# Optimization experiments

Measured on AMD Instinct MI355X. Metric: run time of the kernel, lower is better.

Reference implementation:

```python
import jax, jax.numpy as jnp
import numpy as np

D_MODEL = 768
D_STATE = 128
EXPAND = 2
D_CONV = 4
HEADDIM = 48
D_INNER = EXPAND * D_MODEL            # 1536
NHEADS = D_INNER // HEADDIM           # 32
CONV_DIM = D_INNER + 2 * D_STATE      # 1792 (ngroups=1)
D_IN_PROJ = 2 * D_INNER + 2 * D_STATE + NHEADS  # 3360
EPS = 1e-5


def setup_inputs() -> dict:
    key = jax.random.key(0)
    ks = jax.random.split(key, 8)
    B, L = 2, 1024
    x = jax.random.normal(ks[0], (B, L, D_MODEL), dtype=jnp.float32)
    in_proj_w = jax.random.normal(ks[1], (D_IN_PROJ, D_MODEL), dtype=jnp.float32) * 0.02
    conv_w = jax.random.normal(ks[2], (CONV_DIM, D_CONV), dtype=jnp.float32) * 0.1
    conv_b = jnp.zeros((CONV_DIM,), dtype=jnp.float32)
    # dt init as in Mamba2: dt ~ logspace[1e-3, 1e-1], dt_bias = softplus^-1(dt)
    u = jax.random.uniform(ks[3], (NHEADS,), dtype=jnp.float32)
    dt = jnp.exp(u * (np.log(0.1) - np.log(0.001)) + np.log(0.001))
    dt_bias = jnp.log(jnp.expm1(dt))
    # A in [1, 16]
    A_log = jnp.log(jax.random.uniform(ks[4], (NHEADS,), dtype=jnp.float32) * 15.0 + 1.0)
    D = jnp.ones((NHEADS,), dtype=jnp.float32)
    rms_w = jnp.ones((D_INNER,), dtype=jnp.float32)
    out_proj_w = jax.random.normal(ks[5], (D_MODEL, D_INNER), dtype=jnp.float32) * 0.02
    ln_w = jnp.ones((D_MODEL,), dtype=jnp.float32)
    ln_b = jnp.zeros((D_MODEL,), dtype=jnp.float32)
    return {"x": x, "in_proj_w": in_proj_w, "conv_w": conv_w, "conv_b": conv_b,
            "dt_bias": dt_bias, "A_log": A_log, "D": D, "rms_w": rms_w,
            "out_proj_w": out_proj_w, "ln_w": ln_w, "ln_b": ln_b}


def _mamba_block(x, in_proj_w, conv_w, conv_b, dt_bias, A_log, D, rms_w, out_proj_w, ln_w, ln_b):
    B, L, _ = x.shape
    zxbcdt = jnp.einsum('bld,ed->ble', x, in_proj_w)          # (B,L,D_IN_PROJ)
    z = zxbcdt[..., :D_INNER]                                  # gate
    xBC = zxbcdt[..., D_INNER:D_INNER + CONV_DIM]              # (B,L,CONV_DIM)
    dt = jax.nn.softplus(zxbcdt[..., -NHEADS:] + dt_bias)      # (B,L,H)

    # causal depthwise conv1d (kernel 4) + SiLU
    xp = jnp.pad(xBC, ((0, 0), (D_CONV - 1, 0), (0, 0)))
    conv = conv_b
    for k in range(D_CONV):
        conv = conv + xp[:, k:k + L, :] * conv_w[:, k]
    xBC = jax.nn.silu(conv)

    xs = xBC[..., :D_INNER].reshape(B, L, NHEADS, HEADDIM)     # (B,L,H,P)
    Bm = xBC[..., D_INNER:D_INNER + D_STATE]                   # (B,L,N)
    Cm = xBC[..., D_INNER + D_STATE:]                          # (B,L,N)

    A = -jnp.exp(A_log)                                        # (H,)
    dA = jnp.exp(dt * A)                                       # (B,L,H)
    xdt = xs * dt[..., None]                                   # (B,L,H,P)

    def step(h, inp):
        dA_t, xdt_t, B_t, C_t = inp                            # (B,H),(B,H,P),(B,N),(B,N)
        h = h * dA_t[:, :, None, None] + jnp.einsum('bhp,bn->bhpn', xdt_t, B_t)
        y_t = jnp.einsum('bhpn,bn->bhp', h, C_t)
        return h, y_t

    h0 = jnp.zeros((B, NHEADS, HEADDIM, D_STATE), dtype=x.dtype)
    _, ys = jax.lax.scan(step, h0,
                         (dA.transpose(1, 0, 2), xdt.transpose(1, 0, 2, 3),
                          Bm.transpose(1, 0, 2), Cm.transpose(1, 0, 2)))
    y = ys.transpose(1, 0, 2, 3) + D[None, None, :, None] * xs  # (B,L,H,P)
    y = y.reshape(B, L, D_INNER)

    # gated RMSNorm: rmsnorm(y * silu(z)) * rms_w
    yg = y * jax.nn.silu(z)
    yg = yg * jax.lax.rsqrt(jnp.mean(yg * yg, axis=-1, keepdims=True) + EPS) * rms_w
    out = jnp.einsum('ble,de->bld', yg, out_proj_w)

    # residual + LayerNorm
    r = out + x
    mu = jnp.mean(r, axis=-1, keepdims=True)
    var = jnp.mean((r - mu) ** 2, axis=-1, keepdims=True)
    return (r - mu) * jax.lax.rsqrt(var + EPS) * ln_w + ln_b


def reference(x, in_proj_w, conv_w, conv_b, dt_bias, A_log, D, rms_w, out_proj_w, ln_w, ln_b):
    return _mamba_block(x, in_proj_w, conv_w, conv_b, dt_bias, A_log, D, rms_w,
                        out_proj_w, ln_w, ln_b)
```

## Files before the change

### kernel.cpp

```cpp
#include <hip/hip_runtime.h>
#include <math.h>

#define BDIM 2
#define LLEN 1024
#define DMODEL 768
#define DINNER 1536
#define DSTATE 128
#define NH 32
#define HD 48
#define CONVD 1792
#define DPROJ 3360
#define DPROJP 3456
#define QCH 128
#define NCH 8
#define ROWS (BDIM*LLEN)

typedef unsigned short ushort_t;
typedef __attribute__((ext_vector_type(4))) short short4v;
typedef __attribute__((ext_vector_type(8))) short short8v;
typedef __attribute__((ext_vector_type(4))) float floatx4;

#define OFF_ZX   0ull
#define OFF_XBC  3538944ull
#define OFF_DT   5373952ull
#define OFF_LA   5439488ull
#define OFF_SC   5505024ull
#define OFF_Y    8650752ull
#define OFF_PP   10223616ull
#define OFF_CBT  10224640ull
#define OFF_BTBF 10486784ull
#define OFF_XPT  10617856ull
#define OFF_XBF  12190720ull
#define OFF_IPW  12977152ull
#define OFF_OPW  14304256ull
#define OFF_YBF  14894080ull
#define OFF_GO   16466944ull

__device__ __forceinline__ ushort_t f2bf(float f) {
  union { float f; unsigned int u; } v; v.f = f;
  return (ushort_t)((v.u + 0x7FFFu + ((v.u >> 16) & 1u)) >> 16);
}
__device__ __forceinline__ float bf2f(short s) {
  union { unsigned int u; float f; } v; v.u = ((unsigned int)(ushort_t)s) << 16;
  return v.f;
}

#define GLOAD_LDS16(gptr, lptr) \
  __builtin_amdgcn_global_load_lds( \
      (const __attribute__((address_space(1))) void*)(gptr), \
      (__attribute__((address_space(3))) void*)(lptr), 16, 0, 0)

__global__ __launch_bounds__(256) void convert_in_kernel(
    const float* __restrict__ x, const float* __restrict__ w,
    const float* __restrict__ opw, ushort_t* __restrict__ xbf,
    ushort_t* __restrict__ ipwbf, ushort_t* __restrict__ opwbf) {
  const int blk = blockIdx.x;
  if (blk < 768) {
    const int i = blk * 256 + threadIdx.x;
    const float4 a = ((const float4*)x)[i * 2];
    const float4 b = ((const float4*)x)[i * 2 + 1];
    short8v o;
    o[0] = (short)f2bf(a.x); o[1] = (short)f2bf(a.y);
    o[2] = (short)f2bf(a.z); o[3] = (short)f2bf(a.w);
    o[4] = (short)f2bf(b.x); o[5] = (short)f2bf(b.y);
    o[6] = (short)f2bf(b.z); o[7] = (short)f2bf(b.w);
    *(short8v*)(xbf + (size_t)i * 8) = o;
  } else if (blk < 2064) {
    const int i = (blk - 768) * 256 + threadIdx.x;
    const int row = i / (DMODEL / 8);
    short8v o;
    if (row < DPROJ) {
      const float4 a = ((const float4*)w)[i * 2];
      const float4 b = ((const float4*)w)[i * 2 + 1];
      o[0] = (short)f2bf(a.x); o[1] = (short)f2bf(a.y);
      o[2] = (short)f2bf(a.z); o[3] = (short)f2bf(a.w);
      o[4] = (short)f2bf(b.x); o[5] = (short)f2bf(b.y);
      o[6] = (short)f2bf(b.z); o[7] = (short)f2bf(b.w);
    } else {
      for (int j = 0; j < 8; j++) o[j] = 0;
    }
    *(short8v*)(ipwbf + (size_t)i * 8) = o;
  } else {
    const int i = (blk - 2064) * 256 + threadIdx.x;
    const float4 a = ((const float4*)opw)[i * 2];
    const float4 b = ((const float4*)opw)[i * 2 + 1];
    short8v o;
    o[0] = (short)f2bf(a.x); o[1] = (short)f2bf(a.y);
    o[2] = (short)f2bf(a.z); o[3] = (short)f2bf(a.w);
    o[4] = (short)f2bf(b.x); o[5] = (short)f2bf(b.y);
    o[6] = (short)f2bf(b.z); o[7] = (short)f2bf(b.w);
    *(short8v*)(opwbf + (size_t)i * 8) = o;
  }
}

__global__ __launch_bounds__(256) void gemm_bf16_bfout(
    const ushort_t* __restrict__ A, const ushort_t* __restrict__ B,
    ushort_t* __restrict__ C, int M, int N, int K) {
  __shared__ __align__(16) ushort_t As[128 * 32];
  __shared__ __align__(16) ushort_t Bs[128 * 32];
  const int tid = threadIdx.x, lane = tid & 63, w = tid >> 6;
  const int wm = (w >> 1) * 64, wn = (w & 1) * 64;
  const int m0 = blockIdx.y * 128, n0 = blockIdx.x * 128;
  floatx4 acc[4][4];
#pragma unroll
  for (int i = 0; i < 4; i++)
#pragma unroll
    for (int j = 0; j < 4; j++) acc[i][j] = (floatx4){0.f, 0.f, 0.f, 0.f};
  const int srow = tid >> 2, skc = (tid & 3) * 8;
  const int kk = (lane >> 4) * 8, fr = lane & 15;
  for (int k0 = 0; k0 < K; k0 += 32) {
#pragma unroll
    for (int i = 0; i < 2; i++) {
      GLOAD_LDS16(A + (size_t)(m0 + i * 64 + srow) * K + k0 + skc,
                  As + (i * 64 + srow) * 32 + skc);
      GLOAD_LDS16(B + (size_t)(n0 + i * 64 + srow) * K + k0 + skc,
                  Bs + (i * 64 + srow) * 32 + skc);
    }
    __syncthreads();
    short8v a[4], bv[4];
#pragma unroll
    for (int mr = 0; mr < 4; mr++)
      a[mr] = *(const short8v*)(As + (wm + mr * 16 + fr) * 32 + kk);
#pragma unroll
    for (int nc = 0; nc < 4; nc++)
      bv[nc] = *(const short8v*)(Bs + (wn + nc * 16 + fr) * 32 + kk);
#pragma unroll
    for (int mr = 0; mr < 4; mr++)
#pragma unroll
      for (int nc = 0; nc < 4; nc++)
        acc[mr][nc] = __builtin_amdgcn_mfma_f32_16x16x32_bf16(
            a[mr], bv[nc], acc[mr][nc], 0, 0, 0);
    __syncthreads();
  }
  const int crow = (lane >> 4) * 4;
#pragma unroll
  for (int mr = 0; mr < 4; mr++)
#pragma unroll
    for (int nc = 0; nc < 4; nc++)
#pragma unroll
      for (int j = 0; j < 4; j++)
        C[(size_t)(m0 + wm + mr * 16 + crow + j) * N + n0 + wn + nc * 16 + fr] =
            f2bf(acc[mr][nc][j]);
}

__global__ __launch_bounds__(256) void gemm_bf16_n64(
    const ushort_t* __restrict__ A, const ushort_t* __restrict__ B,
    float* __restrict__ C, int M, int N, int K) {
  __shared__ __align__(16) ushort_t As[128 * 32];
  __shared__ __align__(16) ushort_t Bs[64 * 32];
  const int tid = threadIdx.x, lane = tid & 63, w = tid >> 6;
  const int wm = (w >> 1) * 64, wn = (w & 1) * 32;
  const int m0 = blockIdx.y * 128, n0 = blockIdx.x * 64;
  floatx4 acc[4][2];
#pragma unroll
  for (int i = 0; i < 4; i++)
#pragma unroll
    for (int j = 0; j < 2; j++) acc[i][j] = (floatx4){0.f, 0.f, 0.f, 0.f};
  const int srow = tid >> 2, skc = (tid & 3) * 8;
  const int kk = (lane >> 4) * 8, fr = lane & 15;
  for (int k0 = 0; k0 < K; k0 += 32) {
#pragma unroll
    for (int i = 0; i < 2; i++)
      GLOAD_LDS16(A + (size_t)(m0 + i * 64 + srow) * K + k0 + skc,
                  As + (i * 64 + srow) * 32 + skc);
    GLOAD_LDS16(B + (size_t)(n0 + srow) * K + k0 + skc, Bs + srow * 32 + skc);
    __syncthreads();
    short8v a[4], bv[2];
#pragma unroll
    for (int mr = 0; mr < 4; mr++)
      a[mr] = *(const short8v*)(As + (wm + mr * 16 + fr) * 32 + kk);
#pragma unroll
    for (int nc = 0; nc < 2; nc++)
      bv[nc] = *(const short8v*)(Bs + (wn + nc * 16 + fr) * 32 + kk);
#pragma unroll
    for (int mr = 0; mr < 4; mr++)
#pragma unroll
      for (int nc = 0; nc < 2; nc++)
        acc[mr][nc] = __builtin_amdgcn_mfma_f32_16x16x32_bf16(
            a[mr], bv[nc], acc[mr][nc], 0, 0, 0);
    __syncthreads();
  }
  const int crow = (lane >> 4) * 4;
#pragma unroll
  for (int mr = 0; mr < 4; mr++)
#pragma unroll
    for (int nc = 0; nc < 2; nc++)
#pragma unroll
      for (int j = 0; j < 4; j++)
        C[(size_t)(m0 + wm + mr * 16 + crow + j) * N + n0 + wn + nc * 16 + fr] =
            acc[mr][nc][j];
}

__global__ __launch_bounds__(256) void conv_dt_kernel(
    const ushort_t* __restrict__ zxb, const float* __restrict__ conv_w,
    const float* __restrict__ conv_b, const float* __restrict__ dt_bias,
    ushort_t* __restrict__ xbcb, float* __restrict__ dtbuf) {
  const int row = blockIdx.x;
  const int t = row % LLEN;
  const int tid = threadIdx.x;
  for (int g = tid; g < CONVD / 4; g += 256) {
    const int c = g * 4;
    const float4 cb = *(const float4*)&conv_b[c];
    float acc0 = cb.x, acc1 = cb.y, acc2 = cb.z, acc3 = cb.w;
    float4 cw[4];
#pragma unroll
    for (int j = 0; j < 4; j++) cw[j] = *(const float4*)&conv_w[(c + j) * 4];
#pragma unroll
    for (int k = 0; k < 4; k++) {
      if (t - 3 + k >= 0) {
        const short4v v = *(const short4v*)&zxb[(size_t)(row - 3 + k) * DPROJP + DINNER + c];
        acc0 += bf2f(v[0]) * ((const float*)&cw[0])[k];
        acc1 += bf2f(v[1]) * ((const float*)&cw[1])[k];
        acc2 += bf2f(v[2]) * ((const float*)&cw[2])[k];
        acc3 += bf2f(v[3]) * ((const float*)&cw[3])[k];
      }
    }
    short4v o;
    o[0] = (short)f2bf(acc0 / (1.f + expf(-acc0)));
    o[1] = (short)f2bf(acc1 / (1.f + expf(-acc1)));
    o[2] = (short)f2bf(acc2 / (1.f + expf(-acc2)));
    o[3] = (short)f2bf(acc3 / (1.f + expf(-acc3)));
    *(short4v*)&xbcb[(size_t)row * CONVD + c] = o;
  }
  if (tid < NH) {
    const float v = bf2f(zxb[(size_t)row * DPROJP + (DPROJ - NH) + tid]) + dt_bias[tid];
    dtbuf[row * NH + tid] = (v > 20.f) ? v : log1pf(expf(v));
  }
}

__global__ __launch_bounds__(256) void prepfuse_kernel(
    const ushort_t* __restrict__ xbcb, const float* __restrict__ dtb,
    const float* __restrict__ A_log, ushort_t* __restrict__ XpT,
    ushort_t* __restrict__ BTbf, float* __restrict__ la2,
    float* __restrict__ Pp) {
  __shared__ ushort_t lb[128][136];
  __shared__ float dts[128];
  const int blk = blockIdx.x;
  const int tid = threadIdx.x;
  if (blk < 512) {
    const int c = blk & 7, h = (blk >> 3) & 31, b = blk >> 8;
    const int row0 = b * LLEN + c * QCH;
    if (tid < 128) dts[tid] = dtb[(size_t)(row0 + tid) * NH + h];
    __syncthreads();
    for (int idx = tid; idx < 128 * 12; idx += 256) {
      const int r = idx / 12, f4 = (idx % 12) * 4;
      const short4v v = *(const short4v*)&xbcb[(size_t)(row0 + r) * CONVD + h * HD + f4];
      const float d = dts[r];
      short4v o;
      o[0] = (short)f2bf(bf2f(v[0]) * d); o[1] = (short)f2bf(bf2f(v[1]) * d);
      o[2] = (short)f2bf(bf2f(v[2]) * d); o[3] = (short)f2bf(bf2f(v[3]) * d);
      *(short4v*)&lb[r][f4] = o;
    }
    __syncthreads();
    const size_t base = ((size_t)(b * NCH + c) * NH + h) * HD * 128;
    for (int idx = tid; idx < 48 * 16; idx += 256) {
      const int p = idx % 48, t0 = (idx / 48) * 8;
      short8v o;
#pragma unroll
      for (int j = 0; j < 8; j++) o[j] = lb[t0 + j][p];
      *(short8v*)&XpT[base + (size_t)p * 128 + t0] = o;
    }
  } else if (blk < 528) {
    const int bc = blk - 512;
    const int b = bc / NCH, c = bc % NCH;
    const int row0 = b * LLEN + c * QCH;
    for (int idx = tid; idx < 128 * 32; idx += 256) {
      const int t = idx >> 5, f4 = (idx & 31) * 4;
      const short4v v = *(const short4v*)&xbcb[(size_t)(row0 + t) * CONVD + DINNER + f4];
      *(short4v*)&lb[t][f4] = v;
    }
    __syncthreads();
    for (int idx = tid; idx < 128 * 16; idx += 256) {
      const int n = idx & 127, t0 = (idx >> 7) * 8;
      short8v o;
#pragma unroll
      for (int j = 0; j < 8; j++) o[j] = lb[t0 + j][n];
      *(short8v*)&BTbf[(size_t)(bc * 128 + n) * 128 + t0] = o;
    }
  } else {
    const int idx = blk - 528;
    const int c = idx & 7, h = (idx >> 3) & 31, b = idx >> 8;
    const int lane = tid & 63;
    const int row = b * LLEN + c * QCH + tid;
    float v = 0.f;
    if (tid < 128) v = dtb[(size_t)row * NH + h];
#pragma unroll
    for (int off = 1; off < 64; off <<= 1) {
      const float u = __shfl_up(v, off, 64);
      if (lane >= off) v += u;
    }
    if (tid == 63) dts[0] = v;
    __syncthreads();
    if (tid >= 64 && tid < 128) v += dts[0];
    if (tid < 128) {
      const float la2v = -expf(A_log[h]) * v * 1.44269504088896f;
      la2[(size_t)row * NH + h] = la2v;
      if (tid == 127) Pp[(b * NH + h) * NCH + c] = exp2f(la2v);
    }
  }
}

__global__ __launch_bounds__(256) void stateA_cbt_kernel(
    const ushort_t* __restrict__ XpT, const ushort_t* __restrict__ BTbf,
    const ushort_t* __restrict__ xbcb, const float* __restrict__ la2,
    float* __restrict__ Sc, float* __restrict__ CBt) {
  __shared__ float ew[128];
  const int blk = blockIdx.x;
  const int tid = threadIdx.x, lane = tid & 63, w = tid >> 6;
  const int fr = lane & 15, kk = (lane >> 4) * 8;
  if (blk < 512) {
    const int c = blk & 7, h = (blk >> 3) & 31, b = blk >> 8;
    const int bc = b * NCH + c, bh = b * NH + h;
    const int row0 = b * LLEN + c * QCH;
    const float laL = la2[(size_t)(row0 + 127) * NH + h];
    if (tid < 128) ew[tid] = exp2f(laL - la2[(size_t)(row0 + tid) * NH + h]);
    __syncthreads();
    const int wn = w * 32;
    const size_t xbase = ((size_t)bc * NH + h) * HD * 128;
    floatx4 acc[3][2];
#pragma unroll
    for (int i = 0; i < 3; i++)
#pragma unroll
      for (int j = 0; j < 2; j++) acc[i][j] = (floatx4){0.f, 0.f, 0.f, 0.f};
    for (int ki = 0; ki < 4; ki++) {
      const int kg = ki * 32 + kk;
      short8v a[3], bv[2];
#pragma unroll
      for (int mt = 0; mt < 3; mt++) {
        const short8v raw = *(const short8v*)&XpT[xbase + (size_t)(mt * 16 + fr) * 128 + kg];
        short8v s;
#pragma unroll
        for (int e = 0; e < 8; e++) s[e] = (short)f2bf(bf2f(raw[e]) * ew[kg + e]);
        a[mt] = s;
      }
#pragma unroll
      for (int nt = 0; nt < 2; nt++)
        bv[nt] = *(const short8v*)&BTbf[(size_t)(bc * 128 + wn + nt * 16 + fr) * 128 + kg];
#pragma unroll
      for (int mt = 0; mt < 3; mt++)
#pragma unroll
        for (int nt = 0; nt < 2; nt++)
          acc[mt][nt] = __builtin_amdgcn_mfma_f32_16x16x32_bf16(
              a[mt], bv[nt], acc[mt][nt], 0, 0, 0);
    }
    const int crow = (lane >> 4) * 4;
    float* sc = Sc + (size_t)(bh * NCH + c) * (HD * DSTATE);
#pragma unroll
    for (int mt = 0; mt < 3; mt++)
#pragma unroll
      for (int nt = 0; nt < 2; nt++)
#pragma unroll
        for (int j = 0; j < 4; j++)
          sc[(size_t)(mt * 16 + crow + j) * 128 + wn + nt * 16 + fr] = acc[mt][nt][j];
  } else {
    const int bc = blk - 512;
    const int b = bc / NCH, c = bc % NCH;
    const int row0 = b * LLEN + c * QCH;
    const int wm = w * 32;
    floatx4 acc[2][8];
#pragma unroll
    for (int i = 0; i < 2; i++)
#pragma unroll
      for (int j = 0; j < 8; j++) acc[i][j] = (floatx4){0.f, 0.f, 0.f, 0.f};
    for (int ki = 0; ki < 4; ki++) {
      const int kg = ki * 32 + kk;
      short8v a[2], bv[8];
#pragma unroll
      for (int mt = 0; mt < 2; mt++)
        a[mt] = *(const short8v*)&xbcb[(size_t)(row0 + wm + mt * 16 + fr) * CONVD +
                                       DINNER + DSTATE + kg];
#pragma unroll
      for (int nt = 0; nt < 8; nt++)
        bv[nt] = *(const short8v*)&xbcb[(size_t)(row0 + nt * 16 + fr) * CONVD +
                                        DINNER + kg];
#pragma unroll
      for (int mt = 0; mt < 2; mt++)
#pragma unroll
        for (int nt = 0; nt < 8; nt++)
          acc[mt][nt] = __builtin_amdgcn_mfma_f32_16x16x32_bf16(
              a[mt], bv[nt], acc[mt][nt], 0, 0, 0);
    }
    const int crow = (lane >> 4) * 4;
#pragma unroll
    for (int mt = 0; mt < 2; mt++)
#pragma unroll
      for (int nt = 0; nt < 8; nt++)
#pragma unroll
        for (int j = 0; j < 4; j++)
          CBt[(size_t)(bc * 128 + wm + mt * 16 + crow + j) * 128 + nt * 16 + fr] =
              acc[mt][nt][j];
  }
}

__global__ __launch_bounds__(256) void chunk_combine_kernel(
    float* __restrict__ Sc, const float* __restrict__ Pp) {
  const int bh = blockIdx.x >> 3;
  const int slice = blockIdx.x & 7;
  const int tid = threadIdx.x;
  const int e0 = slice * 768;
  for (int e = e0 + tid; e < e0 + 768; e += 256) {
    float hv = 0.f;
#pragma unroll
    for (int c = 0; c < NCH; c++) {
      const size_t idx = ((size_t)(bh * NCH + c)) * HD * DSTATE + e;
      const float sv = Sc[idx];
      Sc[idx] = hv;
      hv = hv * Pp[bh * NCH + c] + sv;
    }
  }
}

__global__ __launch_bounds__(256) void ykernel(
    const float* __restrict__ CBt, const ushort_t* __restrict__ XpT,
    const ushort_t* __restrict__ xbcb, const float* __restrict__ Hc,
    const float* __restrict__ la2, ushort_t* __restrict__ yb) {
  const int c = blockIdx.x, h = blockIdx.y, b = blockIdx.z;
  const int bc = b * NCH + c, bh = b * NH + h;
  const int row0 = b * LLEN + c * QCH;
  const int tid = threadIdx.x, lane = tid & 63, w = tid >> 6;
  __shared__ float laL[128], el[128];
  if (tid < 128) {
    const float v = la2[(size_t)(row0 + tid) * NH + h];
    laL[tid] = v; el[tid] = exp2f(v);
  }
  __syncthreads();
  const int wm = w * 32;
  const int fr = lane & 15, kk = (lane >> 4) * 8;
  const size_t xbase = ((size_t)bc * NH + h) * HD * 128;
  const float* hin = Hc + (size_t)(bh * NCH + c) * (HD * DSTATE);
  floatx4 acc[2][3];
#pragma unroll
  for (int i = 0; i < 2; i++)
#pragma unroll
    for (int j = 0; j < 3; j++) acc[i][j] = (floatx4){0.f, 0.f, 0.f, 0.f};

  for (int ki = 0; ki < 4; ki++) {
    const int kg = ki * 32 + kk;
    short8v a[2], bv[3];
#pragma unroll
    for (int mt = 0; mt < 2; mt++) {
      const int t = wm + mt * 16 + fr;
      const float lt = laL[t];
      const float* cb = &CBt[(size_t)(bc * 128 + t) * 128 + kg];
      const float4 u0 = *(const float4*)cb;
      const float4 u1 = *(const float4*)(cb + 4);
      const float f[8] = {u0.x, u0.y, u0.z, u0.w, u1.x, u1.y, u1.z, u1.w};
      short8v s;
#pragma unroll
      for (int e = 0; e < 8; e++) {
        const int sidx = kg + e;
        const float m = (t >= sidx) ? exp2f(lt - laL[sidx]) : 0.f;
        s[e] = (short)f2bf(f[e] * m);
      }
      a[mt] = s;
    }
#pragma unroll
    for (int nt = 0; nt < 3; nt++)
      bv[nt] = *(const short8v*)&XpT[xbase + (size_t)(nt * 16 + fr) * 128 + kg];
#pragma unroll
    for (int mt = 0; mt < 2; mt++)
#pragma unroll
      for (int nt = 0; nt < 3; nt++)
        acc[mt][nt] = __builtin_amdgcn_mfma_f32_16x16x32_bf16(
            a[mt], bv[nt], acc[mt][nt], 0, 0, 0);
  }
  for (int ki = 0; ki < 4; ki++) {
    const int kg = ki * 32 + kk;
    short8v a[2], bv[3];
#pragma unroll
    for (int mt = 0; mt < 2; mt++) {
      const int t = wm + mt * 16 + fr;
      const float scl = el[t];
      const short8v raw = *(const short8v*)&xbcb[(size_t)(row0 + t) * CONVD +
                                                 DINNER + DSTATE + kg];
      short8v s;
#pragma unroll
      for (int e = 0; e < 8; e++) s[e] = (short)f2bf(bf2f(raw[e]) * scl);
      a[mt] = s;
    }
#pragma unroll
    for (int nt = 0; nt < 3; nt++) {
      const float* hp = &hin[(size_t)(nt * 16 + fr) * 128 + kg];
      const float4 u0 = *(const float4*)hp;
      const float4 u1 = *(const float4*)(hp + 4);
      const float f[8] = {u0.x, u0.y, u0.z, u0.w, u1.x, u1.y, u1.z, u1.w};
      short8v s;
#pragma unroll
      for (int e = 0; e < 8; e++) s[e] = (short)f2bf(f[e]);
      bv[nt] = s;
    }
#pragma unroll
    for (int mt = 0; mt < 2; mt++)
#pragma unroll
      for (int nt = 0; nt < 3; nt++)
        acc[mt][nt] = __builtin_amdgcn_mfma_f32_16x16x32_bf16(
            a[mt], bv[nt], acc[mt][nt], 0, 0, 0);
  }
  const int crow = (lane >> 4) * 4;
#pragma unroll
  for (int mt = 0; mt < 2; mt++)
#pragma unroll
    for (int nt = 0; nt < 3; nt++)
#pragma unroll
      for (int j = 0; j < 4; j++) {
        const int row = row0 + wm + mt * 16 + crow + j;
        yb[(size_t)row * DINNER + h * HD + nt * 16 + fr] = f2bf(acc[mt][nt][j]);
      }
}

__global__ __launch_bounds__(256) void gate_rms_kernel(
    const ushort_t* __restrict__ zxb, const ushort_t* __restrict__ xbcb,
    const float* __restrict__ Dv, const float* __restrict__ rms_w,
    const ushort_t* __restrict__ yb, ushort_t* __restrict__ ybf) {
  const int row = blockIdx.x;
  const int tid = threadIdx.x;
  __shared__ float sred[4];
  float g[8];
  float ss = 0.f;
  if (tid < 192) {
    const int e0 = tid * 8;
    const short8v xv = *(const short8v*)&xbcb[(size_t)row * CONVD + e0];
    const short8v zv = *(const short8v*)&zxb[(size_t)row * DPROJP + e0];
    const short8v yv = *(const short8v*)&yb[(size_t)row * DINNER + e0];
#pragma unroll
    for (int j = 0; j < 8; j++) {
      const int e = e0 + j;
      const float yf = bf2f(yv[j]) + Dv[e / HD] * bf2f(xv[j]);
      const float z = bf2f(zv[j]);
      const float gv = yf * (z / (1.f + expf(-z)));
      g[j] = gv;
      ss += gv * gv;
    }
  } else {
#pragma unroll
    for (int j = 0; j < 8; j++) g[j] = 0.f;
  }
#pragma unroll
  for (int off = 32; off; off >>= 1) ss += __shfl_down(ss, off, 64);
  if ((tid & 63) == 0) sred[tid >> 6] = ss;
  __syncthreads();
  const float tot = sred[0] + sred[1] + sred[2] + sred[3];
  const float scale = rsqrtf(tot / DINNER + 1e-5f);
  if (tid < 192) {
    const int e0 = tid * 8;
    const float4 w0 = *(const float4*)&rms_w[e0];
    const float4 w1 = *(const float4*)&rms_w[e0 + 4];
    const float wf[8] = {w0.x, w0.y, w0.z, w0.w, w1.x, w1.y, w1.z, w1.w};
    short8v o;
#pragma unroll
    for (int j = 0; j < 8; j++) o[j] = (short)f2bf(g[j] * scale * wf[j]);
    *(short8v*)&ybf[(size_t)row * DINNER + e0] = o;
  }
}

__global__ __launch_bounds__(256) void resid_ln_kernel(
    const float* __restrict__ go, const float* __restrict__ x,
    const float* __restrict__ ln_w, const float* __restrict__ ln_b,
    float* __restrict__ out) {
  const int row = blockIdx.x;
  const int tid = threadIdx.x;
  __shared__ float sred[4];
  __shared__ float sred2[4];
  float r[3];
  float s = 0.f;
#pragma unroll
  for (int i = 0; i < 3; i++) {
    const int e = tid + i * 256;
    r[i] = go[(size_t)row * DMODEL + e] + x[(size_t)row * DMODEL + e];
    s += r[i];
  }
#pragma unroll
  for (int off = 32; off; off >>= 1) s += __shfl_down(s, off, 64);
  if ((tid & 63) == 0) sred[tid >> 6] = s;
  __syncthreads();
  const float mu = (sred[0] + sred[1] + sred[2] + sred[3]) * (1.f / DMODEL);
  float s2 = 0.f;
#pragma unroll
  for (int i = 0; i < 3; i++) {
    const float d = r[i] - mu;
    s2 += d * d;
  }
#pragma unroll
  for (int off = 32; off; off >>= 1) s2 += __shfl_down(s2, off, 64);
  if ((tid & 63) == 0) sred2[tid >> 6] = s2;
  __syncthreads();
  const float var = (sred2[0] + sred2[1] + sred2[2] + sred2[3]) * (1.f / DMODEL);
  const float inv = rsqrtf(var + 1e-5f);
#pragma unroll
  for (int i = 0; i < 3; i++) {
    const int e = tid + i * 256;
    out[(size_t)row * DMODEL + e] = (r[i] - mu) * inv * ln_w[e] + ln_b[e];
  }
}

extern "C" void kernel_launch(void* const* d_in, const int* in_sizes, int n_in,
                              void* d_out, int out_size, void* d_ws, size_t ws_size,
                              hipStream_t stream) {
  const float* x          = (const float*)d_in[0];
  const float* in_proj_w  = (const float*)d_in[1];
  const float* conv_w     = (const float*)d_in[2];
  const float* conv_b     = (const float*)d_in[3];
  const float* dt_bias    = (const float*)d_in[4];
  const float* A_log      = (const float*)d_in[5];
  const float* Dv         = (const float*)d_in[6];
  const float* rms_w      = (const float*)d_in[7];
  const float* out_proj_w = (const float*)d_in[8];
  const float* ln_w       = (const float*)d_in[9];
  const float* ln_b       = (const float*)d_in[10];
  float* out = (float*)d_out;
  float* ws  = (float*)d_ws;

  ushort_t* zxb   = (ushort_t*)(ws + OFF_ZX);
  ushort_t* xbcb  = (ushort_t*)(ws + OFF_XBC);
  float* dtb  = ws + OFF_DT;
  float* la2  = ws + OFF_LA;
  float* Sc   = ws + OFF_SC;
  ushort_t* ybuf = (ushort_t*)(ws + OFF_Y);
  float* Pp   = ws + OFF_PP;
  float* CBt  = ws + OFF_CBT;
  ushort_t* BTbf  = (ushort_t*)(ws + OFF_BTBF);
  ushort_t* XpT   = (ushort_t*)(ws + OFF_XPT);
  ushort_t* xbf   = (ushort_t*)(ws + OFF_XBF);
  ushort_t* ipwbf = (ushort_t*)(ws + OFF_IPW);
  ushort_t* opwbf = (ushort_t*)(ws + OFF_OPW);
  ushort_t* ybf   = (ushort_t*)(ws + OFF_YBF);
  float*    go    = ws + OFF_GO;

  convert_in_kernel<<<2640, 256, 0, stream>>>(x, in_proj_w, out_proj_w,
                                              xbf, ipwbf, opwbf);
  gemm_bf16_bfout<<<dim3(DPROJP / 128, ROWS / 128), 256, 0, stream>>>(
      xbf, ipwbf, zxb, ROWS, DPROJP, DMODEL);
  conv_dt_kernel<<<ROWS, 256, 0, stream>>>(zxb, conv_w, conv_b, dt_bias, xbcb, dtb);
  prepfuse_kernel<<<1040, 256, 0, stream>>>(xbcb, dtb, A_log, XpT, BTbf, la2, Pp);
  stateA_cbt_kernel<<<528, 256, 0, stream>>>(XpT, BTbf, xbcb, la2, Sc, CBt);
  chunk_combine_kernel<<<512, 256, 0, stream>>>(Sc, Pp);
  ykernel<<<dim3(NCH, NH, BDIM), 256, 0, stream>>>(CBt, XpT, xbcb, Sc, la2, ybuf);
  gate_rms_kernel<<<ROWS, 256, 0, stream>>>(zxb, xbcb, Dv, rms_w, ybuf, ybf);
  gemm_bf16_n64<<<dim3(DMODEL / 64, ROWS / 128), 256, 0, stream>>>(
      ybf, opwbf, go, ROWS, DMODEL, DINNER);
  resid_ln_kernel<<<ROWS, 256, 0, stream>>>(go, x, ln_w, ln_b, out);
}
```

Before: 210.0 us.

## Fuse chunk-state combine into ykernel, store CB in bf16, resize blocks

Removes the separate chunk_combine kernel. Each ykernel block now rebuilds its incoming chunk state from the per-chunk states and decay products and stages it in shared memory. The CB matrix is stored as bf16, halving its write and read traffic, at some precision cost. conv_dt and gate_rms launch with block sizes matched to their work (448 and 192 threads), dropping the strided loop and the idle threads. The combine work is redone across chunks per block (up to 7 state reads each), trading one launch and a read-write pass over the states for extra global reads.

```diff
diff --git a/kernel.cpp b/kernel.cpp
--- a/kernel.cpp
+++ b/kernel.cpp
@@ -191,15 +191,15 @@
             acc[mr][nc][j];
 }
 
-__global__ __launch_bounds__(256) void conv_dt_kernel(
+__global__ __launch_bounds__(448) void conv_dt_kernel(
     const ushort_t* __restrict__ zxb, const float* __restrict__ conv_w,
     const float* __restrict__ conv_b, const float* __restrict__ dt_bias,
     ushort_t* __restrict__ xbcb, float* __restrict__ dtbuf) {
   const int row = blockIdx.x;
   const int t = row % LLEN;
   const int tid = threadIdx.x;
-  for (int g = tid; g < CONVD / 4; g += 256) {
-    const int c = g * 4;
+  {
+    const int c = tid * 4;
     const float4 cb = *(const float4*)&conv_b[c];
     float acc0 = cb.x, acc1 = cb.y, acc2 = cb.z, acc3 = cb.w;
     float4 cw[4];
@@ -303,7 +303,7 @@
 __global__ __launch_bounds__(256) void stateA_cbt_kernel(
     const ushort_t* __restrict__ XpT, const ushort_t* __restrict__ BTbf,
     const ushort_t* __restrict__ xbcb, const float* __restrict__ la2,
-    float* __restrict__ Sc, float* __restrict__ CBt) {
+    float* __restrict__ Sc, ushort_t* __restrict__ CBtb) {
   __shared__ float ew[128];
   const int blk = blockIdx.x;
   const int tid = threadIdx.x, lane = tid & 63, w = tid >> 6;
@@ -387,47 +387,56 @@
       for (int nt = 0; nt < 8; nt++)
 #pragma unroll
         for (int j = 0; j < 4; j++)
-          CBt[(size_t)(bc * 128 + wm + mt * 16 + crow + j) * 128 + nt * 16 + fr] =
-              acc[mt][nt][j];
-  }
-}
-
-__global__ __launch_bounds__(256) void chunk_combine_kernel(
-    float* __restrict__ Sc, const float* __restrict__ Pp) {
-  const int bh = blockIdx.x >> 3;
-  const int slice = blockIdx.x & 7;
-  const int tid = threadIdx.x;
-  const int e0 = slice * 768;
-  for (int e = e0 + tid; e < e0 + 768; e += 256) {
-    float hv = 0.f;
-#pragma unroll
-    for (int c = 0; c < NCH; c++) {
-      const size_t idx = ((size_t)(bh * NCH + c)) * HD * DSTATE + e;
-      const float sv = Sc[idx];
-      Sc[idx] = hv;
-      hv = hv * Pp[bh * NCH + c] + sv;
-    }
+          CBtb[(size_t)(bc * 128 + wm + mt * 16 + crow + j) * 128 + nt * 16 + fr] =
+              f2bf(acc[mt][nt][j]);
   }
 }
 
 __global__ __launch_bounds__(256) void ykernel(
-    const float* __restrict__ CBt, const ushort_t* __restrict__ XpT,
-    const ushort_t* __restrict__ xbcb, const float* __restrict__ Hc,
-    const float* __restrict__ la2, ushort_t* __restrict__ yb) {
+    const ushort_t* __restrict__ CBtb, const ushort_t* __restrict__ XpT,
+    const ushort_t* __restrict__ xbcb, const float* __restrict__ Sc,
+    const float* __restrict__ Pp, const float* __restrict__ la2,
+    ushort_t* __restrict__ yb) {
   const int c = blockIdx.x, h = blockIdx.y, b = blockIdx.z;
   const int bc = b * NCH + c, bh = b * NH + h;
   const int row0 = b * LLEN + c * QCH;
   const int tid = threadIdx.x, lane = tid & 63, w = tid >> 6;
   __shared__ float laL[128], el[128];
+  __shared__ float hls[48][132];
   if (tid < 128) {
     const float v = la2[(size_t)(row0 + tid) * NH + h];
     laL[tid] = v; el[tid] = exp2f(v);
+  }
+  {
+    float hacc[24];
+#pragma unroll
+    for (int i = 0; i < 24; i++) hacc[i] = 0.f;
+    float factor = 1.f;
+    const float* scb = Sc + (size_t)bh * NCH * (HD * DSTATE);
+    for (int s = c - 1; s >= 0; --s) {
+      const float* sp = scb + (size_t)s * (HD * DSTATE);
+      const float pf = factor;
+#pragma unroll
+      for (int i = 0; i < 6; i++) {
+        const int e = (tid + i * 256) * 4;
+        const float4 v = *(const float4*)&sp[e];
+        hacc[i * 4 + 0] += pf * v.x; hacc[i * 4 + 1] += pf * v.y;
+        hacc[i * 4 + 2] += pf * v.z; hacc[i * 4 + 3] += pf * v.w;
+      }
+      factor *= Pp[bh * NCH + s];
+    }
+#pragma unroll
+    for (int i = 0; i < 6; i++) {
+      const int e = (tid + i * 256) * 4;
+      const int p = e >> 7, n = e & 127;
+      *(float4*)&hls[p][n] =
+          make_float4(hacc[i * 4], hacc[i * 4 + 1], hacc[i * 4 + 2], hacc[i * 4 + 3]);
+    }
   }
   __syncthreads();
   const int wm = w * 32;
   const int fr = lane & 15, kk = (lane >> 4) * 8;
   const size_t xbase = ((size_t)bc * NH + h) * HD * 128;
-  const float* hin = Hc + (size_t)(bh * NCH + c) * (HD * DSTATE);
   floatx4 acc[2][3];
 #pragma unroll
   for (int i = 0; i < 2; i++)
@@ -441,16 +450,13 @@
     for (int mt = 0; mt < 2; mt++) {
       const int t = wm + mt * 16 + fr;
       const float lt = laL[t];
-      const float* cb = &CBt[(size_t)(bc * 128 + t) * 128 + kg];
-      const float4 u0 = *(const float4*)cb;
-      const float4 u1 = *(const float4*)(cb + 4);
-      const float f[8] = {u0.x, u0.y, u0.z, u0.w, u1.x, u1.y, u1.z, u1.w};
+      const short8v cb = *(const short8v*)&CBtb[(size_t)(bc * 128 + t) * 128 + kg];
       short8v s;
 #pragma unroll
       for (int e = 0; e < 8; e++) {
         const int sidx = kg + e;
         const float m = (t >= sidx) ? exp2f(lt - laL[sidx]) : 0.f;
-        s[e] = (short)f2bf(f[e] * m);
+        s[e] = (short)f2bf(bf2f(cb[e]) * m);
       }
       a[mt] = s;
     }
@@ -480,7 +486,7 @@
     }
 #pragma unroll
     for (int nt = 0; nt < 3; nt++) {
-      const float* hp = &hin[(size_t)(nt * 16 + fr) * 128 + kg];
+      const float* hp = &hls[nt * 16 + fr][kg];
       const float4 u0 = *(const float4*)hp;
       const float4 u1 = *(const float4*)(hp + 4);
       const float f[8] = {u0.x, u0.y, u0.z, u0.w, u1.x, u1.y, u1.z, u1.w};
@@ -508,17 +514,17 @@
       }
 }
 
-__global__ __launch_bounds__(256) void gate_rms_kernel(
+__global__ __launch_bounds__(192) void gate_rms_kernel(
     const ushort_t* __restrict__ zxb, const ushort_t* __restrict__ xbcb,
     const float* __restrict__ Dv, const float* __restrict__ rms_w,
     const ushort_t* __restrict__ yb, ushort_t* __restrict__ ybf) {
   const int row = blockIdx.x;
   const int tid = threadIdx.x;
-  __shared__ float sred[4];
+  __shared__ float sred[3];
   float g[8];
   float ss = 0.f;
-  if (tid < 192) {
-    const int e0 = tid * 8;
+  const int e0 = tid * 8;
+  {
     const short8v xv = *(const short8v*)&xbcb[(size_t)row * CONVD + e0];
     const short8v zv = *(const short8v*)&zxb[(size_t)row * DPROJP + e0];
     const short8v yv = *(const short8v*)&yb[(size_t)row * DINNER + e0];
@@ -531,18 +537,14 @@
       g[j] = gv;
       ss += gv * gv;
     }
-  } else {
-#pragma unroll
-    for (int j = 0; j < 8; j++) g[j] = 0.f;
   }
 #pragma unroll
   for (int off = 32; off; off >>= 1) ss += __shfl_down(ss, off, 64);
   if ((tid & 63) == 0) sred[tid >> 6] = ss;
   __syncthreads();
-  const float tot = sred[0] + sred[1] + sred[2] + sred[3];
+  const float tot = sred[0] + sred[1] + sred[2];
   const float scale = rsqrtf(tot / DINNER + 1e-5f);
-  if (tid < 192) {
-    const int e0 = tid * 8;
+  {
     const float4 w0 = *(const float4*)&rms_w[e0];
     const float4 w1 = *(const float4*)&rms_w[e0 + 4];
     const float wf[8] = {w0.x, w0.y, w0.z, w0.w, w1.x, w1.y, w1.z, w1.w};
@@ -617,7 +619,7 @@
   float* Sc   = ws + OFF_SC;
   ushort_t* ybuf = (ushort_t*)(ws + OFF_Y);
   float* Pp   = ws + OFF_PP;
-  float* CBt  = ws + OFF_CBT;
+  ushort_t* CBtb  = (ushort_t*)(ws + OFF_CBT);
   ushort_t* BTbf  = (ushort_t*)(ws + OFF_BTBF);
   ushort_t* XpT   = (ushort_t*)(ws + OFF_XPT);
   ushort_t* xbf   = (ushort_t*)(ws + OFF_XBF);
@@ -630,12 +632,11 @@
                                               xbf, ipwbf, opwbf);
   gemm_bf16_bfout<<<dim3(DPROJP / 128, ROWS / 128), 256, 0, stream>>>(
       xbf, ipwbf, zxb, ROWS, DPROJP, DMODEL);
-  conv_dt_kernel<<<ROWS, 256, 0, stream>>>(zxb, conv_w, conv_b, dt_bias, xbcb, dtb);
+  conv_dt_kernel<<<ROWS, 448, 0, stream>>>(zxb, conv_w, conv_b, dt_bias, xbcb, dtb);
   prepfuse_kernel<<<1040, 256, 0, stream>>>(xbcb, dtb, A_log, XpT, BTbf, la2, Pp);
-  stateA_cbt_kernel<<<528, 256, 0, stream>>>(XpT, BTbf, xbcb, la2, Sc, CBt);
-  chunk_combine_kernel<<<512, 256, 0, stream>>>(Sc, Pp);
-  ykernel<<<dim3(NCH, NH, BDIM), 256, 0, stream>>>(CBt, XpT, xbcb, Sc, la2, ybuf);
-  gate_rms_kernel<<<ROWS, 256, 0, stream>>>(zxb, xbcb, Dv, rms_w, ybuf, ybf);
+  stateA_cbt_kernel<<<528, 256, 0, stream>>>(XpT, BTbf, xbcb, la2, Sc, CBtb);
+  ykernel<<<dim3(NCH, NH, BDIM), 256, 0, stream>>>(CBtb, XpT, xbcb, Sc, Pp, la2, ybuf);
+  gate_rms_kernel<<<ROWS, 192, 0, stream>>>(zxb, xbcb, Dv, rms_w, ybuf, ybf);
   gemm_bf16_n64<<<dim3(DMODEL / 64, ROWS / 128), 256, 0, stream>>>(
       ybf, opwbf, go, ROWS, DMODEL, DINNER);
   resid_ln_kernel<<<ROWS, 256, 0, stream>>>(go, x, ln_w, ln_b, out);
```

Result: no change. 212.2 us (+1.0%).
